# Performance work log

Hardware: AMD Instinct MI355X
Metric: run time of the kernel (lower is better)

The kernel has to match this reference:

```python
import jax, jax.numpy as jnp
import numpy as np
import math

WINDOW_LEFT = 512   # sliding-window: each query attends to keys in [q-512, q]
WINDOW_RIGHT = 0    # causal
NEG_INF = -1e30


def setup_inputs() -> dict:
    key = jax.random.key(0)
    kq, kk, kv, ks = jax.random.split(key, 4)
    B, S, H, D = 2, 2048, 16, 128
    q = jax.random.normal(kq, (B, S, H, D), dtype=jnp.float32)
    k = jax.random.normal(kk, (B, S, H, D), dtype=jnp.float32)
    v = jax.random.normal(kv, (B, S, H, D), dtype=jnp.float32)
    # geometric-ish ALiBi slopes per head (positive, decaying), like flash-attn
    alibi_slopes = jax.random.uniform(ks, (H,), dtype=jnp.float32, minval=0.001, maxval=0.5)
    return {"q": q, "k": k, "v": v, "alibi_slopes": alibi_slopes}


def reference(q, k, v, alibi_slopes):
    # q,k,v: [B, S, H, D]; alibi_slopes: [H]
    B, S, H, D = q.shape
    scale = 1.0 / math.sqrt(D)
    # scores: [B, H, Sq, Sk]
    scores = jnp.einsum("bqhd,bkhd->bhqk", q, k) * scale
    qi = jnp.arange(S)[:, None]
    ki = jnp.arange(S)[None, :]
    rel = ki - qi  # [Sq, Sk], <=0 for past keys
    # ALiBi bias (equal q/k lengths): -slope * |q - k|
    alibi = -alibi_slopes[:, None, None] * jnp.abs(rel).astype(scores.dtype)  # [H,Sq,Sk]
    scores = scores + alibi[None, :, :, :]
    # causal + sliding-window mask: allow WINDOW_RIGHT future, WINDOW_LEFT past
    mask = (rel <= WINDOW_RIGHT) & (rel >= -WINDOW_LEFT)  # [Sq, Sk]
    scores = jnp.where(mask[None, None, :, :], scores, NEG_INF)
    p = jax.nn.softmax(scores, axis=-1)
    out = jnp.einsum("bhqk,bkhd->bqhd", p, v)
    return out
```

## Files before the change

kernel.cpp:

```cpp
#include <hip/hip_runtime.h>
#include <hip/hip_bf16.h>

typedef __attribute__((ext_vector_type(8))) __bf16 bf16x8;
typedef __attribute__((ext_vector_type(4))) __bf16 bf16x4;
typedef __attribute__((ext_vector_type(2))) __bf16 bf16x2;
typedef __attribute__((ext_vector_type(4))) float f32x4;

#define MFMA32(a, b, c) __builtin_amdgcn_mfma_f32_16x16x32_bf16((a), (b), (c), 0, 0, 0)

constexpr int Bc = 2, Sc = 2048, Hc = 16, Dc = 128;
constexpr int HD = Hc * Dc;
constexpr int QB = 256;
constexpr float SCALE = 0.0883883476483184405f;
constexpr float NEGF = -30000.0f;
constexpr int KSTR = 2080;

__device__ inline bf16x8 cvt8(f32x4 a, f32x4 b) {
    bf16x8 r;
    r[0]=(__bf16)a[0]; r[1]=(__bf16)a[1]; r[2]=(__bf16)a[2]; r[3]=(__bf16)a[3];
    r[4]=(__bf16)b[0]; r[5]=(__bf16)b[1]; r[6]=(__bf16)b[2]; r[7]=(__bf16)b[3];
    return r;
}

__global__ __launch_bounds__(512, 2) void lumen_attn_kernel(
    const float* __restrict__ Q, const float* __restrict__ K,
    const float* __restrict__ V, const float* __restrict__ SLP,
    float* __restrict__ O)
{
    __shared__ __align__(16) char k_lds[2][64 * 256];
    __shared__ __align__(16) char v_lds[2][8 * KSTR];
    __shared__ __align__(16) char p_lds[8][32 * 128];

    const int tid  = threadIdx.x;
    const int lane = tid & 63;
    const int wid  = tid >> 6;
    const int cl = lane & 15;
    const int kg = lane >> 4;
    const int r0 = kg << 2;

    const int bid = blockIdx.x;
    const int swz = (bid & 7) * 32 + (bid >> 3);
    const int qb  = (swz & 7) * QB;
    const int bh  = swz >> 3;
    const int h = bh & 15, b = bh >> 4;

    const float slope = SLP[h];
    const size_t base = (size_t)b * Sc * HD + (size_t)h * Dc;
    const float* qp = Q + base;
    const float* kp = K + base;
    const float* vp = V + base;
    float*       op = O + base;

    const int qw = qb + wid * 32;

    bf16x8 qf[2][4];
    #pragma unroll
    for (int s = 0; s < 2; ++s) {
        const float* qrow = qp + (size_t)(qw + s * 16 + cl) * HD + kg * 8;
        #pragma unroll
        for (int c = 0; c < 4; ++c) {
            f32x4 a = *(const f32x4*)(qrow + c * 32);
            f32x4 bq = *(const f32x4*)(qrow + c * 32 + 4);
            #pragma unroll
            for (int i = 0; i < 4; ++i) { a[i] *= SCALE; bq[i] *= SCALE; }
            qf[s][c] = cvt8(a, bq);
        }
    }

    f32x4 o_acc[2][8];
    #pragma unroll
    for (int s = 0; s < 2; ++s)
        #pragma unroll
        for (int nn = 0; nn < 8; ++nn) o_acc[s][nn] = f32x4{0.f, 0.f, 0.f, 0.f};
    float ssum[2] = {0.f, 0.f};

    int voff[8];
    #pragma unroll
    for (int nn = 0; nn < 8; ++nn) {
        const int d = nn * 16 + cl;
        const int s = (d & ~7) | ((d & 7) ^ ((d >> 3) & 7));
        voff[nn] = s * 16;
    }

    const int kb0    = qb > 512 ? qb - 512 : 0;
    const int kb_end = qb + QB - 64;
    const int NT     = (kb_end - kb0) / 64 + 1;

    const int ktk = tid >> 3;
    const int kd0 = (tid & 7) * 16;
    const int ksw = (ktk & 15) << 4;
    const int vtk = tid >> 4;
    const int vd0 = (tid & 15) * 8;
    const int va_ = tid & 15;

    char* const pw = p_lds[wid];
    const int swp = (cl & 7) << 4;

    f32x4 ra, rb, rc, rd, sa, sb, sc, sd;

    #define LOAD(kbn) do {                                                     \
        const float* kr_ = kp + (size_t)((kbn) + ktk) * HD + kd0;              \
        ra = *(const f32x4*)kr_;        rb = *(const f32x4*)(kr_ + 4);         \
        rc = *(const f32x4*)(kr_ + 8);  rd = *(const f32x4*)(kr_ + 12);        \
        const float* vr_ = vp + (size_t)((kbn) + 2 * vtk) * HD + vd0;          \
        sa = *(const f32x4*)vr_;        sb = *(const f32x4*)(vr_ + 4);         \
        sc = *(const f32x4*)(vr_ + HD); sd = *(const f32x4*)(vr_ + HD + 4);    \
    } while (0)

    #define WRITE(bi) do {                                                     \
        bf16x8 kw0_ = cvt8(ra, rb), kw1_ = cvt8(rc, rd);                       \
        char* kb_ = k_lds[bi] + ktk * 256;                                     \
        *(bf16x8*)(kb_ + ((kd0 * 2) ^ ksw))      = kw0_;                       \
        *(bf16x8*)(kb_ + ((kd0 * 2 + 16) ^ ksw)) = kw1_;                       \
        bf16x8 vw0_ = cvt8(sa, sb), vw1_ = cvt8(sc, sd);                       \
        char* vdst_ = v_lds[bi] + (vtk >> 2) * KSTR + (vtk & 3) * 4;           \
        _Pragma("unroll")                                                      \
        for (int j = 0; j < 8; ++j) {                                          \
            const int s_ = va_ * 8 + (j ^ (va_ & 7));                          \
            bf16x2 pk_; pk_[0] = vw0_[j]; pk_[1] = vw1_[j];                    \
            *(bf16x2*)(vdst_ + s_ * 16) = pk_;                                 \
        }                                                                      \
    } while (0)

    LOAD(kb0);
    WRITE(0);

    for (int i = 0; i < NT; ++i) {
        const int kb  = kb0 + i * 64;
        const int cur = i & 1;
        __syncthreads();

        if (i + 1 < NT) {
            LOAD(kb + 64);
            __builtin_amdgcn_sched_barrier(0);
        }

        if (!(kb > qw + 31 || kb + 63 < qw - 512)) {
            const char* kbuf = k_lds[cur];
            const char* vbuf = v_lds[cur];

            #pragma unroll
            for (int n = 0; n < 4; ++n) {
                f32x4 s0 = f32x4{0.f, 0.f, 0.f, 0.f};
                f32x4 s1 = f32x4{0.f, 0.f, 0.f, 0.f};
                const char* kbse = kbuf + (n * 16 + cl) * 256;
                const int sw = cl << 4;
                #pragma unroll
                for (int c = 0; c < 4; ++c) {
                    bf16x8 kf = *(const bf16x8*)(kbse + (((c * 32 + kg * 8) * 2) ^ sw));
                    s0 = MFMA32(kf, qf[0][c], s0);
                    s1 = MFMA32(kf, qf[1][c], s1);
                }
                const int poff = ((n * 16 + r0) * 2) ^ swp;
                #pragma unroll
                for (int s2 = 0; s2 < 2; ++s2) {
                    const f32x4 sv = s2 ? s1 : s0;
                    const int q = qw + s2 * 16 + cl;
                    bf16x4 pk;
                    #pragma unroll
                    for (int j = 0; j < 4; ++j) {
                        const int rel = q - (kb + n * 16 + r0 + j);
                        const float val = ((unsigned)rel <= 512u)
                                          ? fmaf(-slope, (float)rel, sv[j]) : NEGF;
                        const float pe = __expf(val);
                        ssum[s2] += pe;
                        pk[j] = (__bf16)pe;
                    }
                    *(bf16x4*)(pw + (s2 * 16 + cl) * 128 + poff) = pk;
                }
            }

            asm volatile("s_waitcnt lgkmcnt(0)" ::: "memory");

            #pragma unroll
            for (int kk = 0; kk < 2; ++kk) {
                const int off = ((kk * 32 + kg * 8) * 2) ^ swp;
                bf16x8 pa0 = *(const bf16x8*)(pw + cl * 128 + off);
                bf16x8 pa1 = *(const bf16x8*)(pw + (16 + cl) * 128 + off);
                const char* vko = vbuf + (kk * 4 + kg) * KSTR;
                #pragma unroll
                for (int nn = 0; nn < 8; ++nn) {
                    bf16x8 vf = *(const bf16x8*)(vko + voff[nn]);
                    o_acc[0][nn] = MFMA32(pa0, vf, o_acc[0][nn]);
                    o_acc[1][nn] = MFMA32(pa1, vf, o_acc[1][nn]);
                }
            }
        }

        if (i + 1 < NT) {
            __builtin_amdgcn_sched_barrier(0);
            WRITE(cur ^ 1);
        }
    }

    #pragma unroll
    for (int s = 0; s < 2; ++s) {
        ssum[s] += __shfl_xor(ssum[s], 16);
        ssum[s] += __shfl_xor(ssum[s], 32);
    }
    #pragma unroll
    for (int s = 0; s < 2; ++s) {
        #pragma unroll
        for (int j = 0; j < 4; ++j) {
            const float sj = __shfl(ssum[s], r0 + j);
            const float inv = 1.0f / sj;
            float* orow = op + (size_t)(qw + s * 16 + r0 + j) * HD;
            #pragma unroll
            for (int nn = 0; nn < 8; ++nn)
                orow[nn * 16 + cl] = o_acc[s][nn][j] * inv;
        }
    }
    #undef LOAD
    #undef WRITE
}

extern "C" void kernel_launch(void* const* d_in, const int* in_sizes, int n_in,
                              void* d_out, int out_size, void* d_ws, size_t ws_size,
                              hipStream_t stream) {
    const float* q   = (const float*)d_in[0];
    const float* k   = (const float*)d_in[1];
    const float* v   = (const float*)d_in[2];
    const float* slp = (const float*)d_in[3];
    float* out = (float*)d_out;

    dim3 grid(Bc * Hc * (Sc / QB));
    lumen_attn_kernel<<<grid, dim3(512), 0, stream>>>(q, k, v, slp, out);
}
```

Measured before the change: 47.89 us.

## Permute K rows in LDS so P stays in registers, skipping LDS round-trip

```diff
diff --git a/kernel.cpp b/kernel.cpp
--- a/kernel.cpp
+++ b/kernel.cpp
@@ -2,7 +2,6 @@
 #include <hip/hip_bf16.h>
 
 typedef __attribute__((ext_vector_type(8))) __bf16 bf16x8;
-typedef __attribute__((ext_vector_type(4))) __bf16 bf16x4;
 typedef __attribute__((ext_vector_type(2))) __bf16 bf16x2;
 typedef __attribute__((ext_vector_type(4))) float f32x4;
 
@@ -11,7 +10,8 @@
 constexpr int Bc = 2, Sc = 2048, Hc = 16, Dc = 128;
 constexpr int HD = Hc * Dc;
 constexpr int QB = 256;
-constexpr float SCALE = 0.0883883476483184405f;
+constexpr float SCALE_L2 = (float)(0.08838834764831844 * 1.4426950408889634);
+constexpr float LOG2E = 1.4426950408889634f;
 constexpr float NEGF = -30000.0f;
 constexpr int KSTR = 2080;
 
@@ -29,14 +29,12 @@
 {
     __shared__ __align__(16) char k_lds[2][64 * 256];
     __shared__ __align__(16) char v_lds[2][8 * KSTR];
-    __shared__ __align__(16) char p_lds[8][32 * 128];
 
     const int tid  = threadIdx.x;
     const int lane = tid & 63;
     const int wid  = tid >> 6;
     const int cl = lane & 15;
     const int kg = lane >> 4;
-    const int r0 = kg << 2;
 
     const int bid = blockIdx.x;
     const int swz = (bid & 7) * 32 + (bid >> 3);
@@ -44,7 +42,7 @@
     const int bh  = swz >> 3;
     const int h = bh & 15, b = bh >> 4;
 
-    const float slope = SLP[h];
+    const float slope = SLP[h] * LOG2E;
     const size_t base = (size_t)b * Sc * HD + (size_t)h * Dc;
     const float* qp = Q + base;
     const float* kp = K + base;
@@ -62,7 +60,7 @@
             f32x4 a = *(const f32x4*)(qrow + c * 32);
             f32x4 bq = *(const f32x4*)(qrow + c * 32 + 4);
             #pragma unroll
-            for (int i = 0; i < 4; ++i) { a[i] *= SCALE; bq[i] *= SCALE; }
+            for (int i = 0; i < 4; ++i) { a[i] *= SCALE_L2; bq[i] *= SCALE_L2; }
             qf[s][c] = cvt8(a, bq);
         }
     }
@@ -88,13 +86,12 @@
 
     const int ktk = tid >> 3;
     const int kd0 = (tid & 7) * 16;
-    const int ksw = (ktk & 15) << 4;
+    const int kpos = (2 * ((ktk >> 5) & 1) + ((ktk >> 2) & 1)) * 16
+                   + ((ktk >> 3) & 3) * 4 + (ktk & 3);
+    const int ksw = (kpos & 15) << 4;
     const int vtk = tid >> 4;
     const int vd0 = (tid & 15) * 8;
     const int va_ = tid & 15;
-
-    char* const pw = p_lds[wid];
-    const int swp = (cl & 7) << 4;
 
     f32x4 ra, rb, rc, rd, sa, sb, sc, sd;
 
@@ -109,7 +106,7 @@
 
     #define WRITE(bi) do {                                                     \
         bf16x8 kw0_ = cvt8(ra, rb), kw1_ = cvt8(rc, rd);                       \
-        char* kb_ = k_lds[bi] + ktk * 256;                                     \
+        char* kb_ = k_lds[bi] + kpos * 256;                                    \
         *(bf16x8*)(kb_ + ((kd0 * 2) ^ ksw))      = kw0_;                       \
         *(bf16x8*)(kb_ + ((kd0 * 2 + 16) ^ ksw)) = kw1_;                       \
         bf16x8 vw0_ = cvt8(sa, sb), vw1_ = cvt8(sc, sd);                       \
@@ -139,6 +136,7 @@
             const char* kbuf = k_lds[cur];
             const char* vbuf = v_lds[cur];
 
+            bf16x8 pa[2][2];
             #pragma unroll
             for (int n = 0; n < 4; ++n) {
                 f32x4 s0 = f32x4{0.f, 0.f, 0.f, 0.f};
@@ -151,38 +149,31 @@
                     s0 = MFMA32(kf, qf[0][c], s0);
                     s1 = MFMA32(kf, qf[1][c], s1);
                 }
-                const int poff = ((n * 16 + r0) * 2) ^ swp;
+                const int keyb = kb + kg * 8 + (n & 1) * 4 + ((n >> 1) << 5);
                 #pragma unroll
                 for (int s2 = 0; s2 < 2; ++s2) {
                     const f32x4 sv = s2 ? s1 : s0;
                     const int q = qw + s2 * 16 + cl;
-                    bf16x4 pk;
                     #pragma unroll
                     for (int j = 0; j < 4; ++j) {
-                        const int rel = q - (kb + n * 16 + r0 + j);
+                        const int rel = q - (keyb + j);
                         const float val = ((unsigned)rel <= 512u)
                                           ? fmaf(-slope, (float)rel, sv[j]) : NEGF;
-                        const float pe = __expf(val);
+                        const float pe = exp2f(val);
                         ssum[s2] += pe;
-                        pk[j] = (__bf16)pe;
+                        pa[s2][n >> 1][(n & 1) * 4 + j] = (__bf16)pe;
                     }
-                    *(bf16x4*)(pw + (s2 * 16 + cl) * 128 + poff) = pk;
                 }
             }
 
-            asm volatile("s_waitcnt lgkmcnt(0)" ::: "memory");
-
             #pragma unroll
             for (int kk = 0; kk < 2; ++kk) {
-                const int off = ((kk * 32 + kg * 8) * 2) ^ swp;
-                bf16x8 pa0 = *(const bf16x8*)(pw + cl * 128 + off);
-                bf16x8 pa1 = *(const bf16x8*)(pw + (16 + cl) * 128 + off);
                 const char* vko = vbuf + (kk * 4 + kg) * KSTR;
                 #pragma unroll
                 for (int nn = 0; nn < 8; ++nn) {
                     bf16x8 vf = *(const bf16x8*)(vko + voff[nn]);
-                    o_acc[0][nn] = MFMA32(pa0, vf, o_acc[0][nn]);
-                    o_acc[1][nn] = MFMA32(pa1, vf, o_acc[1][nn]);
+                    o_acc[0][nn] = MFMA32(pa[0][kk], vf, o_acc[0][nn]);
+                    o_acc[1][nn] = MFMA32(pa[1][kk], vf, o_acc[1][nn]);
                 }
             }
         }
@@ -193,6 +184,7 @@
         }
     }
 
+    const int r0 = kg << 2;
     #pragma unroll
     for (int s = 0; s < 2; ++s) {
         ssum[s] += __shfl_xor(ssum[s], 16);
```

Measured after the change: 48.93 us. +2.2%, slower.
